# Kernel optimization log

Hardware: AMD Instinct MI355X
Metric: run time of the kernel (lower is better)

## Reference

```python
import jax, jax.numpy as jnp
import numpy as np

N_NODES = 10000
N_EDGES = 160000
NUM_FEAT = 14
EDGE_DIM = 4
DIM = 64        # hidden_channels
HID = 128       # GENConv MLP expansion = 2
LAYERS = 28
MSG_EPS = 1e-7  # GENConv eps added to relu(message)
LN_EPS = 1e-5   # torch LayerNorm default


def layernorm(h, g, b):
    mu = jnp.mean(h, axis=-1, keepdims=True)
    var = jnp.mean(jnp.square(h - mu), axis=-1, keepdims=True)
    return (h - mu) * jax.lax.rsqrt(var + LN_EPS) * g + b


def gen_conv(x, ea, src, dst, t, W1, b1, g1, be1, W2, b2):
    # message: relu(x_j + edge_attr) + eps  -> [E, D]
    msg = jax.nn.relu(x[src] + ea) + MSG_EPS
    # softmax aggregation over edges grouped by destination node
    logits = msg * t
    m = jax.ops.segment_max(logits, dst, num_segments=N_NODES)
    e = jnp.exp(logits - m[dst])
    s = jax.ops.segment_sum(e, dst, num_segments=N_NODES)
    alpha = e / (s[dst] + 1e-16)
    agg = jax.ops.segment_sum(msg * alpha, dst, num_segments=N_NODES)
    # residual + MLP [D -> 2D -> D] with LayerNorm+ReLU in between
    h = agg + x
    h = jax.nn.relu(layernorm(h @ W1 + b1, g1, be1))
    return h @ W2 + b2


def setup_inputs() -> dict:
    key = jax.random.key(0)
    ks = jax.random.split(key, 24)
    sc = 0.05
    inp = {
        "x": jax.random.normal(ks[0], (N_NODES, NUM_FEAT), jnp.float32),
        "edge_attr": jax.random.normal(ks[1], (N_EDGES, EDGE_DIM), jnp.float32),
        "src": jax.random.randint(ks[2], (N_EDGES,), 0, N_NODES, jnp.int32),
        "dst": jax.random.randint(ks[3], (N_EDGES,), 0, N_NODES, jnp.int32),
        # encoders
        "W_node": jax.random.normal(ks[4], (NUM_FEAT, DIM), jnp.float32) * sc,
        "b_node": jnp.zeros((DIM,), jnp.float32),
        "W_edge": jax.random.normal(ks[5], (EDGE_DIM, DIM), jnp.float32) * sc,
        "b_edge": jnp.zeros((DIM,), jnp.float32),
        # per-layer GENConv params (stacked over LAYERS)
        "t": jnp.ones((LAYERS,), jnp.float32),
        "W1": jax.random.normal(ks[6], (LAYERS, DIM, HID), jnp.float32) * sc,
        "b1": jnp.zeros((LAYERS, HID), jnp.float32),
        "g1": jnp.ones((LAYERS, HID), jnp.float32),
        "be1": jnp.zeros((LAYERS, HID), jnp.float32),
        "W2": jax.random.normal(ks[7], (LAYERS, HID, DIM), jnp.float32) * sc,
        "b2": jnp.zeros((LAYERS, DIM), jnp.float32),
        # per-layer DeepGCNLayer LayerNorm
        "ln_g": jnp.ones((LAYERS, DIM), jnp.float32),
        "ln_b": jnp.zeros((LAYERS, DIM), jnp.float32),
        # output projection
        "W_out": jax.random.normal(ks[8], (DIM, DIM), jnp.float32) * sc,
        "b_out": jnp.zeros((DIM,), jnp.float32),
    }
    return inp


def reference(x, edge_attr, src, dst, W_node, b_node, W_edge, b_edge,
              t, W1, b1, g1, be1, W2, b2, ln_g, ln_b, W_out, b_out):
    h = x @ W_node + b_node                  # node encoder  [N, D]
    ea = edge_attr @ W_edge + b_edge         # edge encoder  [E, D]

    # layer 0: conv only (no res+ wrapper), per DeeperGCN.forward
    h = gen_conv(h, ea, src, dst, t[0], W1[0], b1[0], g1[0], be1[0], W2[0], b2[0])

    # layers 1..L-1: res+ block: x + conv(dropout(relu(norm(x))))  (eval: dropout = id)
    def step(hc, p):
        ti, w1, bb1, gg1, bbe1, w2, bb2, lg, lb = p
        u = jax.nn.relu(layernorm(hc, lg, lb))
        u = gen_conv(u, ea, src, dst, ti, w1, bb1, gg1, bbe1, w2, bb2)
        return hc + u, None

    rest = (t[1:], W1[1:], b1[1:], g1[1:], be1[1:], W2[1:], b2[1:], ln_g[1:], ln_b[1:])
    h, _ = jax.lax.scan(step, h, rest)

    # final: act(layers[0].norm(x)), dropout (eval: id), lin
    h = jax.nn.relu(layernorm(h, ln_g[0], ln_b[0]))
    return h @ W_out + b_out
```

## Files before the change

### kernel.cpp

```cpp
#include <hip/hip_runtime.h>

#define N_NODES 10000
#define N_EDGES 160000
#define NUM_FEAT 14
#define EDGE_DIM 4
#define DIM 64
#define HID 128
#define LAYERS 28

#define NEG_INF (-__builtin_inff())

__device__ __forceinline__ void stage16(const float* gsrc, float* lds_base) {
  __builtin_amdgcn_global_load_lds(
      (const __attribute__((address_space(1))) void*)gsrc,
      (__attribute__((address_space(3))) void*)lds_base, 16, 0, 0);
}


__global__ __launch_bounds__(256) void k_hist(const int* __restrict__ dst, int* __restrict__ cur) {
  int e = blockIdx.x * 256 + threadIdx.x;
  if (e < N_EDGES) atomicAdd(&cur[dst[e]], 1);
}

__global__ __launch_bounds__(256) void k_scan(int* __restrict__ cur, int* __restrict__ off) {
  __shared__ int part[256];
  int t = threadIdx.x;
  const int CH = 40;
  int base = t * CH;
  int s = 0;
  for (int i = 0; i < CH; i++) {
    int idx = base + i;
    if (idx < N_NODES) s += cur[idx];
  }
  part[t] = s;
  __syncthreads();
  for (int ofs = 1; ofs < 256; ofs <<= 1) {
    int tmp = (t >= ofs) ? part[t - ofs] : 0;
    __syncthreads();
    part[t] += tmp;
    __syncthreads();
  }
  int run = part[t] - s;
  for (int i = 0; i < CH; i++) {
    int idx = base + i;
    if (idx < N_NODES) {
      int d = cur[idx];
      off[idx] = run;
      cur[idx] = run;
      run += d;
    }
  }
  if (t == 255) off[N_NODES] = part[255];
}

__global__ __launch_bounds__(256) void k_scatter(const int* __restrict__ dst, int* __restrict__ cur,
                                                 int* __restrict__ eids) {
  int e = blockIdx.x * 256 + threadIdx.x;
  if (e < N_EDGES) {
    int p = atomicAdd(&cur[dst[e]], 1);
    eids[p] = e;
  }
}

__global__ __launch_bounds__(256) void k_sortgather(
    const int* __restrict__ off, const int* __restrict__ eids,
    const int* __restrict__ src, const float4* __restrict__ eattr,
    const float* __restrict__ W_edge, const float* __restrict__ b_edge,
    int* __restrict__ src_s, float4* __restrict__ eattr_s, float* __restrict__ ea_s) {
  int node = blockIdx.x * 4 + (threadIdx.x >> 6);
  int lane = threadIdx.x & 63;
  if (node >= N_NODES) return;
  float we0 = W_edge[lane], we1 = W_edge[64 + lane], we2 = W_edge[128 + lane],
        we3 = W_edge[192 + lane];
  float be = b_edge[lane];
  int a = off[node];
  int d = off[node + 1] - a;
  if (d <= 64) {
    int key = (lane < d) ? eids[a + lane] : 0x7fffffff;
#pragma unroll
    for (int k = 2; k <= 64; k <<= 1) {
      for (int j = k >> 1; j > 0; j >>= 1) {
        int p = __shfl_xor(key, j);
        bool dirUp = ((lane & k) == 0);
        bool isLower = ((lane & j) == 0);
        key = ((isLower == dirUp) ? min(key, p) : max(key, p));
      }
    }
    float4 ev = make_float4(0.f, 0.f, 0.f, 0.f);
    if (lane < d) {
      src_s[a + lane] = src[key];
      ev = eattr[key];
    }
    for (int j = 0; j < d; j++) {
      float ex = __shfl(ev.x, j), ey = __shfl(ev.y, j),
            ez = __shfl(ev.z, j), ew = __shfl(ev.w, j);
      ea_s[(size_t)(a + j) * 64 + lane] =
          be + ex * we0 + ey * we1 + ez * we2 + ew * we3;
    }
  } else {
    for (int i = lane; i < d; i += 64) {
      int e = eids[a + i];
      int r = 0;
      for (int j = 0; j < d; j++) r += (eids[a + j] < e) ? 1 : 0;
      src_s[a + r] = src[e];
      eattr_s[a + r] = eattr[e];
    }
    for (int j = 0; j < d; j++) {
      float4 e4 = eattr_s[a + j];
      ea_s[(size_t)(a + j) * 64 + lane] =
          be + e4.x * we0 + e4.y * we1 + e4.z * we2 + e4.w * we3;
    }
  }
}


__global__ __launch_bounds__(256) void k_enc(const float* __restrict__ x, const float* __restrict__ Wn,
                                             const float* __restrict__ bn, float* __restrict__ hc,
                                             float* __restrict__ u) {
  int gid = blockIdx.x * 256 + threadIdx.x;
  if (gid >= N_NODES * DIM) return;
  int n = gid >> 6, j = gid & 63;
  float acc = bn[j];
#pragma unroll
  for (int k = 0; k < NUM_FEAT; k++) acc += x[n * NUM_FEAT + k] * Wn[k * DIM + j];
  hc[gid] = acc;
  u[gid] = acc;
}


__global__ __launch_bounds__(256) void k_edge(
    const float* __restrict__ uin, const float* __restrict__ ea_s,
    const int* __restrict__ src_s, const int* __restrict__ off,
    const float* __restrict__ tptr, int layer, float* __restrict__ htmp) {
  int node = __builtin_amdgcn_readfirstlane((blockIdx.x << 2) + (threadIdx.x >> 6));
  int lane = threadIdx.x & 63;
  float tv = tptr[layer];
  int a = off[node], d = off[node + 1] - a;
  float un = uin[(node << 6) + lane];
  float s0 = 0.f, s1 = 0.f, ac0 = 0.f, ac1 = 0.f;
  int i = 0;
  for (; i + 8 <= d; i += 8) {
    float uv[8], ev[8];
#pragma unroll
    for (int j = 0; j < 8; j++) {
      int sn = src_s[a + i + j];
      uv[j] = uin[(sn << 6) + lane];
      ev[j] = ea_s[(size_t)(a + i + j) * 64 + lane];
    }
#pragma unroll
    for (int j = 0; j < 8; j++) {
      float msg = fmaxf(uv[j] + ev[j], 0.f) + 1e-7f;
      float e = __expf(msg * tv);
      if (j & 1) {
        s1 += e;
        ac1 = fmaf(e, msg, ac1);
      } else {
        s0 += e;
        ac0 = fmaf(e, msg, ac0);
      }
    }
  }
  for (; i < d; i++) {
    int sn = src_s[a + i];
    float msg = fmaxf(uin[(sn << 6) + lane] + ea_s[(size_t)(a + i) * 64 + lane], 0.f) + 1e-7f;
    float e = __expf(msg * tv);
    s0 += e;
    ac0 = fmaf(e, msg, ac0);
  }
  float sum = s0 + s1, acc = ac0 + ac1;
  htmp[(node << 6) + lane] = acc / (sum + 1e-16f) + un;
}


#define MBLK (N_NODES / 16)

__global__ __launch_bounds__(512, 4) void k_mlp2(
    const float* __restrict__ hin, float* __restrict__ hc, float* __restrict__ uout,
    const float* __restrict__ W1, const float* __restrict__ b1,
    const float* __restrict__ g1, const float* __restrict__ be1,
    const float* __restrict__ W2, const float* __restrict__ b2,
    const float* __restrict__ lng, const float* __restrict__ lnb,
    int addRes, int writeU) {
  __shared__ float sW1[64 * 128];
  __shared__ float sW2[128 * 64];
  __shared__ float sH[8][128];
  __shared__ float sZ[8][256];

  int tid = threadIdx.x;
  int lane = tid & 63;
  int wv = tid >> 6;
  int gn0 = blockIdx.x * 16 + wv * 2;
  int gn1 = gn0 + 1;

  {
    const float* w1s = W1 + wv * 1024;
    const float* w2s = W2 + wv * 1024;
    float* d1 = sW1 + wv * 1024;
    float* d2 = sW2 + wv * 1024;
#pragma unroll
    for (int r = 0; r < 4; r++) {
      stage16(w1s + r * 256 + lane * 4, d1 + r * 256);
      stage16(w2s + r * 256 + lane * 4, d2 + r * 256);
    }
  }

  {
    float h0 = hin[gn0 * 64 + lane];
    float h1 = hin[gn1 * 64 + lane];
    *((float2*)&sH[wv][lane * 2]) = make_float2(h0, h1);
  }
  __syncthreads();

  int j0 = 2 * lane;
  float2 b1v = *((const float2*)&b1[j0]);
  float a00 = b1v.x, a01 = b1v.y, a10 = b1v.x, a11 = b1v.y;
#pragma unroll 8
  for (int k = 0; k < 64; k++) {
    float2 hp = *((float2*)&sH[wv][k * 2]);
    float2 wp = *((float2*)&sW1[k * 128 + j0]);
    a00 += hp.x * wp.x; a01 += hp.x * wp.y;
    a10 += hp.y * wp.x; a11 += hp.y * wp.y;
  }

  {
    float2 gv = *((const float2*)&g1[j0]);
    float2 bev = *((const float2*)&be1[j0]);
    float s0 = a00 + a01, q0 = a00 * a00 + a01 * a01;
    float s1 = a10 + a11, q1 = a10 * a10 + a11 * a11;
#pragma unroll
    for (int o = 32; o; o >>= 1) {
      s0 += __shfl_xor(s0, o); q0 += __shfl_xor(q0, o);
      s1 += __shfl_xor(s1, o); q1 += __shfl_xor(q1, o);
    }
    float mu0 = s0 * (1.f / 128.f), mu1 = s1 * (1.f / 128.f);
    float rs0 = rsqrtf(q0 * (1.f / 128.f) - mu0 * mu0 + 1e-5f);
    float rs1 = rsqrtf(q1 * (1.f / 128.f) - mu1 * mu1 + 1e-5f);
    float4 zv;
    zv.x = fmaxf((a00 - mu0) * rs0 * gv.x + bev.x, 0.f);
    zv.y = fmaxf((a10 - mu1) * rs1 * gv.x + bev.x, 0.f);
    zv.z = fmaxf((a01 - mu0) * rs0 * gv.y + bev.y, 0.f);
    zv.w = fmaxf((a11 - mu1) * rs1 * gv.y + bev.y, 0.f);
    *((float4*)&sZ[wv][4 * lane]) = zv;
  }

  float bo = b2[lane];
  float o0 = bo, o1 = bo;
#pragma unroll 8
  for (int k = 0; k < 128; k++) {
    float2 zp = *((float2*)&sZ[wv][k * 2]);
    float wv2 = sW2[k * 64 + lane];
    o0 += zp.x * wv2;
    o1 += zp.y * wv2;
  }

  float r0 = addRes ? hc[gn0 * 64 + lane] : 0.f;
  float r1 = addRes ? hc[gn1 * 64 + lane] : 0.f;
  float hcn0 = o0 + r0, hcn1 = o1 + r1;
  hc[gn0 * 64 + lane] = hcn0;
  hc[gn1 * 64 + lane] = hcn1;

  if (writeU) {
    float lg_ = lng[lane], lb_ = lnb[lane];
    float s0 = hcn0, q0 = hcn0 * hcn0;
    float s1 = hcn1, q1 = hcn1 * hcn1;
#pragma unroll
    for (int o = 32; o; o >>= 1) {
      s0 += __shfl_xor(s0, o); q0 += __shfl_xor(q0, o);
      s1 += __shfl_xor(s1, o); q1 += __shfl_xor(q1, o);
    }
    float mu0 = s0 * (1.f / 64.f), mu1 = s1 * (1.f / 64.f);
    float rs0 = rsqrtf(q0 * (1.f / 64.f) - mu0 * mu0 + 1e-5f);
    float rs1 = rsqrtf(q1 * (1.f / 64.f) - mu1 * mu1 + 1e-5f);
    uout[gn0 * 64 + lane] = fmaxf((hcn0 - mu0) * rs0 * lg_ + lb_, 0.f);
    uout[gn1 * 64 + lane] = fmaxf((hcn1 - mu1) * rs1 * lg_ + lb_, 0.f);
  }
}


__global__ __launch_bounds__(256) void k_final(const float* __restrict__ hc, const float* __restrict__ g,
                                               const float* __restrict__ bptr, const float* __restrict__ Wout,
                                               const float* __restrict__ bout, float* __restrict__ out) {
  __shared__ float sW[DIM * DIM];
  int tid = threadIdx.x;
  for (int i = tid; i < 1024; i += 256) ((float4*)sW)[i] = ((const float4*)Wout)[i];
  __syncthreads();
  int lane = tid & 63, w = tid >> 6;
  int n = blockIdx.x * 4 + w;
  if (n >= N_NODES) return;
  float v = hc[n * 64 + lane];
  float s = v, q = v * v;
#pragma unroll
  for (int o = 32; o; o >>= 1) { s += __shfl_xor(s, o); q += __shfl_xor(q, o); }
  float mu = s * (1.f / 64.f);
  float var = q * (1.f / 64.f) - mu * mu;
  float rs = rsqrtf(var + 1e-5f);
  float z = fmaxf((v - mu) * rs * g[lane] + bptr[lane], 0.f);
  float acc = bout[lane];
  for (int k = 0; k < 64; k++) {
    float zk = __shfl(z, k);
    acc += zk * sW[k * 64 + lane];
  }
  out[n * 64 + lane] = acc;
}


extern "C" void kernel_launch(void* const* d_in, const int* in_sizes, int n_in,
                              void* d_out, int out_size, void* d_ws, size_t ws_size,
                              hipStream_t stream) {
  const float* x        = (const float*)d_in[0];
  const float* eattr    = (const float*)d_in[1];
  const int*   src      = (const int*)d_in[2];
  const int*   dst      = (const int*)d_in[3];
  const float* W_node   = (const float*)d_in[4];
  const float* b_node   = (const float*)d_in[5];
  const float* W_edge   = (const float*)d_in[6];
  const float* b_edge   = (const float*)d_in[7];
  const float* t        = (const float*)d_in[8];
  const float* W1       = (const float*)d_in[9];
  const float* b1       = (const float*)d_in[10];
  const float* g1       = (const float*)d_in[11];
  const float* be1      = (const float*)d_in[12];
  const float* W2       = (const float*)d_in[13];
  const float* b2       = (const float*)d_in[14];
  const float* ln_g     = (const float*)d_in[15];
  const float* ln_b     = (const float*)d_in[16];
  const float* W_out    = (const float*)d_in[17];
  const float* b_out    = (const float*)d_in[18];
  float* out = (float*)d_out;

  char* w = (char*)d_ws;
  float* u       = (float*)w;  w += (size_t)N_NODES * 64 * 4;
  float* hcb     = (float*)w;  w += (size_t)N_NODES * 64 * 4;
  float* htmp    = (float*)w;  w += (size_t)N_NODES * 64 * 4;
  int* off       = (int*)w;    w += (size_t)(N_NODES + 1) * 4;
  int* cur       = (int*)w;    w += (size_t)N_NODES * 4;
  int* eids      = (int*)w;    w += (size_t)N_EDGES * 4;
  int* src_s     = (int*)w;    w += (size_t)N_EDGES * 4;
  float4* eattr_s = (float4*)w; w += (size_t)N_EDGES * 16;
  float* ea_s    = (float*)w;  w += (size_t)N_EDGES * 64 * 4;

  hipMemsetAsync(cur, 0, (size_t)N_NODES * 4, stream);
  k_hist<<<(N_EDGES + 255) / 256, 256, 0, stream>>>(dst, cur);
  k_scan<<<1, 256, 0, stream>>>(cur, off);
  k_scatter<<<(N_EDGES + 255) / 256, 256, 0, stream>>>(dst, cur, eids);
  k_sortgather<<<(N_NODES + 3) / 4, 256, 0, stream>>>(off, eids, src, (const float4*)eattr,
                                                      W_edge, b_edge, src_s, eattr_s, ea_s);

  k_enc<<<(N_NODES * 64 + 255) / 256, 256, 0, stream>>>(x, W_node, b_node, hcb, u);

  for (int l = 0; l < LAYERS; l++) {
    k_edge<<<(N_NODES + 3) / 4, 256, 0, stream>>>(u, ea_s, src_s, off, t, l, htmp);
    int nxt = (l + 1 < LAYERS) ? (l + 1) : 0;
    k_mlp2<<<MBLK, 512, 0, stream>>>(htmp, hcb, u,
                                     W1 + (size_t)l * DIM * HID, b1 + (size_t)l * HID,
                                     g1 + (size_t)l * HID, be1 + (size_t)l * HID,
                                     W2 + (size_t)l * HID * DIM, b2 + (size_t)l * DIM,
                                     ln_g + (size_t)nxt * DIM, ln_b + (size_t)nxt * DIM,
                                     (l > 0) ? 1 : 0, (l < LAYERS - 1) ? 1 : 0);
  }

  k_final<<<(N_NODES + 3) / 4, 256, 0, stream>>>(hcb, ln_g, ln_b, W_out, b_out, out);
}
```

Measured before the change: 988.9 us.

## Fuse edge aggregation into per-layer MLP kernel with ping-pong node buffers

Merges the per-node softmax aggregation kernel into the MLP kernel, so each 640-thread block (10 waves) aggregates 20 nodes into shared memory and then runs the MLP on them. This removes the htmp round trip through global memory and halves the number of launches per layer. The u buffers alternate between layers to avoid read/write hazards. In exchange, the weight staging into LDS now overlaps the gather phase, but the larger block size with heavy LDS use may cut occupancy, and the irregular per-node degrees can leave waves idle at the barrier.

Result: faster. 925.4 us (-6.4%).

```diff
diff --git a/kernel.cpp b/kernel.cpp
--- a/kernel.cpp
+++ b/kernel.cpp
@@ -7,8 +7,6 @@
 #define DIM 64
 #define HID 128
 #define LAYERS 28
-
-#define NEG_INF (-__builtin_inff())
 
 __device__ __forceinline__ void stage16(const float* gsrc, float* lds_base) {
   __builtin_amdgcn_global_load_lds(
@@ -128,54 +126,13 @@
 }
 
 
-__global__ __launch_bounds__(256) void k_edge(
-    const float* __restrict__ uin, const float* __restrict__ ea_s,
-    const int* __restrict__ src_s, const int* __restrict__ off,
-    const float* __restrict__ tptr, int layer, float* __restrict__ htmp) {
-  int node = __builtin_amdgcn_readfirstlane((blockIdx.x << 2) + (threadIdx.x >> 6));
-  int lane = threadIdx.x & 63;
-  float tv = tptr[layer];
-  int a = off[node], d = off[node + 1] - a;
-  float un = uin[(node << 6) + lane];
-  float s0 = 0.f, s1 = 0.f, ac0 = 0.f, ac1 = 0.f;
-  int i = 0;
-  for (; i + 8 <= d; i += 8) {
-    float uv[8], ev[8];
-#pragma unroll
-    for (int j = 0; j < 8; j++) {
-      int sn = src_s[a + i + j];
-      uv[j] = uin[(sn << 6) + lane];
-      ev[j] = ea_s[(size_t)(a + i + j) * 64 + lane];
-    }
-#pragma unroll
-    for (int j = 0; j < 8; j++) {
-      float msg = fmaxf(uv[j] + ev[j], 0.f) + 1e-7f;
-      float e = __expf(msg * tv);
-      if (j & 1) {
-        s1 += e;
-        ac1 = fmaf(e, msg, ac1);
-      } else {
-        s0 += e;
-        ac0 = fmaf(e, msg, ac0);
-      }
-    }
-  }
-  for (; i < d; i++) {
-    int sn = src_s[a + i];
-    float msg = fmaxf(uin[(sn << 6) + lane] + ea_s[(size_t)(a + i) * 64 + lane], 0.f) + 1e-7f;
-    float e = __expf(msg * tv);
-    s0 += e;
-    ac0 = fmaf(e, msg, ac0);
-  }
-  float sum = s0 + s1, acc = ac0 + ac1;
-  htmp[(node << 6) + lane] = acc / (sum + 1e-16f) + un;
-}
-
-
-#define MBLK (N_NODES / 16)
-
-__global__ __launch_bounds__(512, 4) void k_mlp2(
-    const float* __restrict__ hin, float* __restrict__ hc, float* __restrict__ uout,
+#define NPB 20
+#define NLB (N_NODES / NPB)
+
+__global__ __launch_bounds__(640, 5) void k_layer(
+    const float* __restrict__ uin, float* __restrict__ hc, float* __restrict__ uout,
+    const float* __restrict__ ea_s, const int* __restrict__ src_s,
+    const int* __restrict__ off, const float* __restrict__ tptr, int layer,
     const float* __restrict__ W1, const float* __restrict__ b1,
     const float* __restrict__ g1, const float* __restrict__ be1,
     const float* __restrict__ W2, const float* __restrict__ b2,
@@ -183,33 +140,66 @@
     int addRes, int writeU) {
   __shared__ float sW1[64 * 128];
   __shared__ float sW2[128 * 64];
-  __shared__ float sH[8][128];
-  __shared__ float sZ[8][256];
-
-  int tid = threadIdx.x;
-  int lane = tid & 63;
-  int wv = tid >> 6;
-  int gn0 = blockIdx.x * 16 + wv * 2;
-  int gn1 = gn0 + 1;
+  __shared__ float sH[10][128];
+  __shared__ float sZ[10][256];
+
+  const int tid = threadIdx.x;
+  const int lane = tid & 63;
+  const int wv = tid >> 6;
+  const int nbase = blockIdx.x * NPB;
+
+  for (int c = wv; c < 32; c += 10) {
+    stage16(W1 + c * 256 + lane * 4, sW1 + c * 256);
+    stage16(W2 + c * 256 + lane * 4, sW2 + c * 256);
+  }
 
   {
-    const float* w1s = W1 + wv * 1024;
-    const float* w2s = W2 + wv * 1024;
-    float* d1 = sW1 + wv * 1024;
-    float* d2 = sW2 + wv * 1024;
-#pragma unroll
-    for (int r = 0; r < 4; r++) {
-      stage16(w1s + r * 256 + lane * 4, d1 + r * 256);
-      stage16(w2s + r * 256 + lane * 4, d2 + r * 256);
-    }
-  }
-
-  {
-    float h0 = hin[gn0 * 64 + lane];
-    float h1 = hin[gn1 * 64 + lane];
-    *((float2*)&sH[wv][lane * 2]) = make_float2(h0, h1);
+    float tv = tptr[layer];
+    float hpair[2];
+#pragma unroll
+    for (int q = 0; q < 2; q++) {
+      int gn = __builtin_amdgcn_readfirstlane(nbase + wv * 2 + q);
+      int a = off[gn], d = off[gn + 1] - a;
+      float un = uin[(gn << 6) + lane];
+      float s0 = 0.f, s1 = 0.f, ac0 = 0.f, ac1 = 0.f;
+      int i = 0;
+      for (; i + 8 <= d; i += 8) {
+        float uv[8], ev[8];
+#pragma unroll
+        for (int j = 0; j < 8; j++) {
+          int sn = src_s[a + i + j];
+          uv[j] = uin[(sn << 6) + lane];
+          ev[j] = ea_s[(size_t)(a + i + j) * 64 + lane];
+        }
+#pragma unroll
+        for (int j = 0; j < 8; j++) {
+          float msg = fmaxf(uv[j] + ev[j], 0.f) + 1e-7f;
+          float e = __expf(msg * tv);
+          if (j & 1) {
+            s1 += e;
+            ac1 = fmaf(e, msg, ac1);
+          } else {
+            s0 += e;
+            ac0 = fmaf(e, msg, ac0);
+          }
+        }
+      }
+      for (; i < d; i++) {
+        int sn = src_s[a + i];
+        float msg = fmaxf(uin[(sn << 6) + lane] + ea_s[(size_t)(a + i) * 64 + lane],
+                          0.f) + 1e-7f;
+        float e = __expf(msg * tv);
+        s0 += e;
+        ac0 = fmaf(e, msg, ac0);
+      }
+      hpair[q] = (ac0 + ac1) / (s0 + s1 + 1e-16f) + un;
+    }
+    *((float2*)&sH[wv][lane * 2]) = make_float2(hpair[0], hpair[1]);
   }
   __syncthreads();
+
+  const int gn0 = nbase + wv * 2;
+  const int gn1 = gn0 + 1;
 
   int j0 = 2 * lane;
   float2 b1v = *((const float2*)&b1[j0]);
@@ -329,9 +319,9 @@
   float* out = (float*)d_out;
 
   char* w = (char*)d_ws;
-  float* u       = (float*)w;  w += (size_t)N_NODES * 64 * 4;
+  float* uA      = (float*)w;  w += (size_t)N_NODES * 64 * 4;
+  float* uB      = (float*)w;  w += (size_t)N_NODES * 64 * 4;
   float* hcb     = (float*)w;  w += (size_t)N_NODES * 64 * 4;
-  float* htmp    = (float*)w;  w += (size_t)N_NODES * 64 * 4;
   int* off       = (int*)w;    w += (size_t)(N_NODES + 1) * 4;
   int* cur       = (int*)w;    w += (size_t)N_NODES * 4;
   int* eids      = (int*)w;    w += (size_t)N_EDGES * 4;
@@ -346,12 +336,13 @@
   k_sortgather<<<(N_NODES + 3) / 4, 256, 0, stream>>>(off, eids, src, (const float4*)eattr,
                                                       W_edge, b_edge, src_s, eattr_s, ea_s);
 
-  k_enc<<<(N_NODES * 64 + 255) / 256, 256, 0, stream>>>(x, W_node, b_node, hcb, u);
+  k_enc<<<(N_NODES * 64 + 255) / 256, 256, 0, stream>>>(x, W_node, b_node, hcb, uA);
 
   for (int l = 0; l < LAYERS; l++) {
-    k_edge<<<(N_NODES + 3) / 4, 256, 0, stream>>>(u, ea_s, src_s, off, t, l, htmp);
+    const float* uin = (l & 1) ? uB : uA;
+    float* uo        = (l & 1) ? uA : uB;
     int nxt = (l + 1 < LAYERS) ? (l + 1) : 0;
-    k_mlp2<<<MBLK, 512, 0, stream>>>(htmp, hcb, u,
+    k_layer<<<NLB, 640, 0, stream>>>(uin, hcb, uo, ea_s, src_s, off, t, l,
                                      W1 + (size_t)l * DIM * HID, b1 + (size_t)l * HID,
                                      g1 + (size_t)l * HID, be1 + (size_t)l * HID,
                                      W2 + (size_t)l * HID * DIM, b2 + (size_t)l * DIM,
```
